# Kernel optimization log

Hardware: AMD Instinct MI355X
Metric: run time of the kernel (lower is better)

The kernel has to match this reference:

```python
import jax, jax.numpy as jnp
import numpy as np

N = 256          # num agents
HID = 128        # hidden_dim
ACT = 5          # action_dim
NH = 4           # num_heads
D = HID + 16     # concat_hidden_dim = 144
E = D * NH       # mha embed dim = 576
HD = D           # per-head dim = E // NH = 144
OBS_RX, OBS_RY = 4, 2   # obs_r from fov_size=(9,5)
GRID = 40


def setup_inputs() -> dict:
    key = jax.random.key(0)
    ks = jax.random.split(key, 24)
    g = lambda k, shape, s: (jax.random.normal(k, shape, dtype=jnp.float32) * s)
    inp = {
        "hidden_state_n": g(ks[0], (N, HID), 1.0),
        "action_n": g(ks[1], (N, HID), 1.0),
        "state_n": jax.random.randint(ks[2], (N, 2), 0, GRID, dtype=jnp.int32),
        # obs encoder
        "W_enc": g(ks[3], (HID, 16), HID ** -0.5), "b_enc": jnp.zeros((16,), jnp.float32),
        # MHABlock outer projections
        "Wq": g(ks[4], (D, E), D ** -0.5), "bq": jnp.zeros((E,), jnp.float32),
        "Wk": g(ks[5], (D, E), D ** -0.5), "bk": jnp.zeros((E,), jnp.float32),
        "Wv": g(ks[6], (D, E), D ** -0.5), "bv": jnp.zeros((E,), jnp.float32),
        # nn.MultiheadAttention internal in/out projections
        "Wiq": g(ks[7], (E, E), E ** -0.5), "biq": jnp.zeros((E,), jnp.float32),
        "Wik": g(ks[8], (E, E), E ** -0.5), "bik": jnp.zeros((E,), jnp.float32),
        "Wiv": g(ks[9], (E, E), E ** -0.5), "biv": jnp.zeros((E,), jnp.float32),
        "Wo_proj": g(ks[10], (E, E), E ** -0.5), "bo_proj": jnp.zeros((E,), jnp.float32),
        "W_O": g(ks[11], (E, D), E ** -0.5),  # no bias
        # dueling decoders
        "W_val": g(ks[12], (D, 1), D ** -0.5), "b_val": jnp.zeros((1,), jnp.float32),
        "W_adv": g(ks[13], (D, ACT), D ** -0.5), "b_adv": jnp.zeros((ACT,), jnp.float32),
    }
    return inp


def reference(hidden_state_n, action_n, W_enc, b_enc, Wq, bq, Wk, bk, Wv, bv,
              Wiq, biq, Wik, bik, Wiv, biv, Wo_proj, bo_proj, W_O,
              W_val, b_val, W_adv, b_adv, state_n):
    n = hidden_state_n.shape[0]
    # observed_agents[i] = {j > i : |x_i-x_j|<=rx and |y_i-y_j|<=ry}
    pos = state_n.astype(jnp.int32)
    dx = jnp.abs(pos[:, None, 0] - pos[None, :, 0])
    dy = jnp.abs(pos[:, None, 1] - pos[None, :, 1])
    upper = jnp.arange(n)[None, :] > jnp.arange(n)[:, None]
    mask = (dx <= OBS_RX) & (dy <= OBS_RY) & upper            # [N,N], mask[i,j]: j observed by i

    # per-neighbor feature c_j = concat(obs_encoder(h_j), a_j)  -> [N, D]
    obs = hidden_state_n @ W_enc + b_enc                       # [N,16]
    C = jnp.concatenate([obs, action_n], axis=-1)              # [N,D]

    # MHABlock: outer Q/K/V projections then nn.MultiheadAttention
    q = (C @ Wq + bq) @ Wiq + biq                              # [N,E]
    k = (C @ Wk + bk) @ Wik + bik
    v = (C @ Wv + bv) @ Wiv + biv
    q2 = q.reshape(n, NH, HD)
    k2 = k.reshape(n, NH, HD)
    v2 = v.reshape(n, NH, HD)

    scale = 1.0 / np.sqrt(HD).astype(np.float32)
    S = jnp.einsum("jhd,khd->hjk", q2, k2) * scale             # [H,N,N] shared across agents

    pair = (mask[:, None, :, None] & mask[:, None, None, :])   # [N,1,Nq,Nk]
    logits = jnp.where(pair, S[None, :, :, :], -1e9)           # [N,H,N,N]
    m = jnp.max(logits, axis=-1, keepdims=True)
    p = jnp.exp(logits - m) * pair.astype(logits.dtype)
    attn = p / jnp.maximum(p.sum(axis=-1, keepdims=True), 1e-9)

    ctx = jnp.einsum("ihjk,khd->ijhd", attn, v2).reshape(n, n, E)  # [N,Nq,E]
    out = (ctx @ Wo_proj + bo_proj) @ W_O                          # [N,Nq,D]

    # sum over the (masked) neighbor/query axis -> per-agent h_i
    h = jnp.sum(out * mask[:, :, None].astype(out.dtype), axis=1)  # [N,D]

    V = h @ W_val + b_val                                          # [N,1]
    A = h @ W_adv + b_adv                                          # [N,ACT]
    Q = V + A - jnp.mean(A, axis=-1, keepdims=True)                # dueling Q
    return Q
```

## Files before the change

kernel.cpp:

```cpp
#include <hip/hip_runtime.h>
#include <hip/hip_bf16.h>

#define NAG 256
#define HID 128
#define ACT 5
#define NH 4
#define DD 144
#define EE 576
#define HDIM 144
#define CMAX 20

__device__ __forceinline__ void prod_tile(
    const float* __restrict__ A, const float* __restrict__ W,
    float* __restrict__ out, int rowbase, int colbase, int N,
    int tid, float* sm)
{
    const int LDA = 580;
    float* As = sm;
    for (int idx = tid; idx < 8 * 144; idx += 256) {
        int r = idx / 144, c = idx % 144;
        *((float4*)&As[r * LDA + c * 4]) =
            *(const float4*)(A + (size_t)(rowbase + r) * 576 + c * 4);
    }
    __syncthreads();
    const int wave = tid >> 6, lane = tid & 63;
    const int colg = colbase + lane;
    const int colc = (colg < N) ? colg : (N - 1);
    const float* Wp = W + (size_t)(wave * 144) * N + colc;
    float acc[8] = {};
    float wv[36], wn[36];
    #pragma unroll
    for (int j = 0; j < 36; ++j) wv[j] = Wp[(size_t)j * N];
    for (int gi = 0; gi < 4; ++gi) {
        if (gi + 1 < 4) {
            const float* Wn = Wp + (size_t)(gi + 1) * 36 * N;
            #pragma unroll
            for (int j = 0; j < 36; ++j) wn[j] = Wn[(size_t)j * N];
        }
        const int kb = wave * 144 + gi * 36;
        #pragma unroll
        for (int j4 = 0; j4 < 9; ++j4) {
            #pragma unroll
            for (int r = 0; r < 8; ++r) {
                float4 a4 = *(const float4*)&As[r * LDA + kb + j4 * 4];
                acc[r] += a4.x * wv[j4 * 4 + 0] + a4.y * wv[j4 * 4 + 1]
                        + a4.z * wv[j4 * 4 + 2] + a4.w * wv[j4 * 4 + 3];
            }
        }
        #pragma unroll
        for (int j = 0; j < 36; ++j) wv[j] = wn[j];
    }
    __syncthreads();
    float* red = sm;
    #pragma unroll
    for (int r = 0; r < 8; ++r) red[wave * 512 + r * 64 + lane] = acc[r];
    __syncthreads();
    #pragma unroll
    for (int q = 0; q < 2; ++q) {
        int idx = tid + q * 256;
        int r = idx >> 6, cl = idx & 63;
        int col = colbase + cl;
        if (col < N) {
            float s = red[idx] + red[512 + idx] + red[1024 + idx] + red[1536 + idx];
            out[(size_t)(rowbase + r) * N + col] = s;
        }
    }
}

__global__ __launch_bounds__(256) void k_pre(
    const float* __restrict__ hidden, const float* __restrict__ action,
    const float* __restrict__ W_enc, const float* __restrict__ b_enc,
    const float* __restrict__ Wq, const float* __restrict__ Wk, const float* __restrict__ Wv,
    const float* __restrict__ bq, const float* __restrict__ bk, const float* __restrict__ bv,
    const float* __restrict__ Wiq, const float* __restrict__ Wik, const float* __restrict__ Wiv,
    const float* __restrict__ biq, const float* __restrict__ bik, const float* __restrict__ biv,
    const float* __restrict__ Wo, const float* __restrict__ bo, const float* __restrict__ W_O,
    float* __restrict__ C,
    float* __restrict__ Wqc, float* __restrict__ Wkc, float* __restrict__ Wvc,
    float* __restrict__ Wc,
    float* __restrict__ bqc, float* __restrict__ bkc, float* __restrict__ bvc,
    float* __restrict__ bvec)
{
    __shared__ float sm[4640];
    const int p = blockIdx.x, tid = threadIdx.x;
    if (p < 576) {
        const int xcd = p & 7, r = p >> 3;
        const int gslot = r / 18, mb = r % 18;
        const int g = xcd + 8 * gslot;
        if (g >= 27) return;
        const int bx = g % 9, z = g / 9;
        const float* A = (z == 0) ? Wq  : (z == 1) ? Wk  : Wv;
        const float* W = (z == 0) ? Wiq : (z == 1) ? Wik : Wiv;
        float*     out = (z == 0) ? Wqc : (z == 1) ? Wkc : Wvc;
        prod_tile(A, W, out, mb * 8, bx * 64, EE, tid, sm);
    } else if (p < 1152) {
        const int pp = p - 576;
        const int xcd = pp & 7, mb = pp >> 3;
        if (xcd >= 3) return;
        prod_tile(Wo, W_O, Wc, mb * 8, xcd * 64, DD, tid, sm);
    } else if (p < 1184) {
        const int mb = p - 1152;
        float* Hs = sm;
        float* We = sm + 1056;
        {
            int r = tid >> 5, kq = tid & 31;
            *((float4*)&Hs[r * 132 + kq * 4]) =
                *(const float4*)(hidden + (mb * 8 + r) * HID + kq * 4);
            float4 a4 = *(const float4*)(action + (mb * 8 + r) * HID + kq * 4);
            *((float4*)(C + (size_t)(mb * 8 + r) * DD + 16 + kq * 4)) = a4;
            *((float4*)&We[tid * 4])        = *(const float4*)(W_enc + tid * 4);
            *((float4*)&We[1024 + tid * 4]) = *(const float4*)(W_enc + 1024 + tid * 4);
        }
        __syncthreads();
        if (tid < 128) {
            int r = tid >> 4, o = tid & 15;
            float acc = 0.f;
            #pragma unroll 8
            for (int d = 0; d < HID; ++d) acc += Hs[r * 132 + d] * We[d * 16 + o];
            C[(size_t)(mb * 8 + r) * DD + o] = acc + b_enc[o];
        }
    } else {
        const int t = p - 1184;
        const float *bsel, *W, *badd;
        float* out;
        int N, bx;
        if (t < 27) {
            int z = t / 9; bx = t % 9; N = EE;
            bsel = (z == 0) ? bq  : (z == 1) ? bk  : bv;
            W    = (z == 0) ? Wiq : (z == 1) ? Wik : Wiv;
            badd = (z == 0) ? biq : (z == 1) ? bik : biv;
            out  = (z == 0) ? bqc : (z == 1) ? bkc : bvc;
        } else {
            bx = t - 27; N = DD;
            bsel = bo; W = W_O; badd = nullptr; out = bvec;
        }
        float* bs = sm;
        float* red = sm + 576;
        for (int i = tid; i < 144; i += 256)
            *((float4*)&bs[i * 4]) = *(const float4*)(bsel + i * 4);
        __syncthreads();
        const int wave = tid >> 6, lane = tid & 63;
        const int colg = bx * 64 + lane;
        const int colc = (colg < N) ? colg : (N - 1);
        float acc = 0.f;
        for (int k = wave * 144; k < wave * 144 + 144; ++k)
            acc += bs[k] * W[(size_t)k * N + colc];
        red[wave * 64 + lane] = acc;
        __syncthreads();
        if (tid < 64 && bx * 64 + tid < N) {
            float s = red[tid] + red[64 + tid] + red[128 + tid] + red[192 + tid];
            out[bx * 64 + tid] = s + (badd ? badd[bx * 64 + tid] : 0.f);
        }
    }
}

__global__ __launch_bounds__(256) void k_qkv(
    const float* __restrict__ C,
    const float* __restrict__ Wqc, const float* __restrict__ Wkc, const float* __restrict__ Wvc,
    const float* __restrict__ bqc, const float* __restrict__ bkc, const float* __restrict__ bvc,
    float* __restrict__ q, float* __restrict__ kb, float* __restrict__ v)
{
    const int p = blockIdx.x;
    const int xcd = p & 7, qq = p >> 3;
    const int mb = qq & 31, gslot = qq >> 5;
    const int g = xcd + 8 * gslot;
    if (g >= 27) return;
    const int bx = g % 9, z = g / 9;
    const float* W  = (z == 0) ? Wqc : (z == 1) ? Wkc : Wvc;
    const float* bi = (z == 0) ? bqc : (z == 1) ? bkc : bvc;
    float*      out = (z == 0) ? q   : (z == 1) ? kb  : v;
    const int tid = threadIdx.x;

    __shared__ union { float As[8 * 148]; float red[2048]; } u;
    for (int idx = tid; idx < 8 * 36; idx += 256) {
        int r = idx / 36, c = idx % 36;
        *((float4*)&u.As[r * 148 + c * 4]) =
            *(const float4*)(C + (size_t)(mb * 8 + r) * DD + c * 4);
    }
    __syncthreads();
    const int wave = tid >> 6, lane = tid & 63;
    const int colg = bx * 64 + lane;
    const float* Wp = W + (size_t)(wave * 36) * EE + colg;
    float acc[8] = {};
    float wv[36];
    #pragma unroll
    for (int j = 0; j < 36; ++j) wv[j] = Wp[(size_t)j * EE];
    const int kbase = wave * 36;
    #pragma unroll
    for (int j4 = 0; j4 < 9; ++j4) {
        #pragma unroll
        for (int r = 0; r < 8; ++r) {
            float4 a4 = *(const float4*)&u.As[r * 148 + kbase + j4 * 4];
            acc[r] += a4.x * wv[j4 * 4 + 0] + a4.y * wv[j4 * 4 + 1]
                    + a4.z * wv[j4 * 4 + 2] + a4.w * wv[j4 * 4 + 3];
        }
    }
    __syncthreads();
    #pragma unroll
    for (int r = 0; r < 8; ++r) u.red[wave * 512 + r * 64 + lane] = acc[r];
    __syncthreads();
    #pragma unroll
    for (int qi = 0; qi < 2; ++qi) {
        int idx = tid + qi * 256;
        int r = idx >> 6, cl = idx & 63;
        int col = bx * 64 + cl;
        float s = u.red[idx] + u.red[512 + idx]
                + u.red[1024 + idx] + u.red[1536 + idx];
        out[(size_t)(mb * 8 + r) * EE + col] = s + bi[col];
    }
}

__global__ __launch_bounds__(256) void k_attn(
    const int* __restrict__ state, const float* __restrict__ q,
    const float* __restrict__ kmat, const float* __restrict__ v,
    float* __restrict__ ctxsum, float* __restrict__ cnt)
{
    __shared__ int lst[NAG];
    __shared__ int cnt_s;
    __shared__ float w4[NH][NAG];
    __shared__ float qh[CMAX][HDIM + 1];
    __shared__ float kh[CMAX][HDIM + 1];
    __shared__ float Sl[CMAX][CMAX + 1];
    const int i = blockIdx.x, tid = threadIdx.x;
    if (tid == 0) cnt_s = 0;
    __syncthreads();
    {
        int xi = state[2 * i], yi = state[2 * i + 1];
        int xj = state[2 * tid], yj = state[2 * tid + 1];
        int dx = xi - xj; if (dx < 0) dx = -dx;
        int dy = yi - yj; if (dy < 0) dy = -dy;
        if (tid > i && dx <= 4 && dy <= 2) {
            int p = atomicAdd(&cnt_s, 1);
            lst[p] = tid;
        }
    }
    __syncthreads();
    const int c = cnt_s;
    if (tid == 0) cnt[i] = (float)c;
    if (c == 0) {
        for (int e = tid; e < EE; e += 256) ctxsum[i * EE + e] = 0.f;
        return;
    }
    if (c <= CMAX) {
        for (int h = 0; h < NH; ++h) {
            for (int idx = tid; idx < c * HDIM; idx += 256) {
                int jj = idx / HDIM, d = idx % HDIM;
                qh[jj][d] = q[lst[jj] * EE + h * HDIM + d];
                kh[jj][d] = kmat[lst[jj] * EE + h * HDIM + d];
            }
            __syncthreads();
            for (int pp = tid; pp < c * c; pp += 256) {
                int jj = pp / c, kk = pp % c;
                float acc = 0.f;
                for (int d = 0; d < HDIM; ++d) acc += qh[jj][d] * kh[kk][d];
                Sl[jj][kk] = acc * (1.0f / 12.0f);
            }
            __syncthreads();
            if (tid < c) {
                float m = -1e30f;
                for (int kk = 0; kk < c; ++kk) m = fmaxf(m, Sl[tid][kk]);
                float zz = 0.f;
                for (int kk = 0; kk < c; ++kk) zz += __expf(Sl[tid][kk] - m);
                float inv = 1.f / fmaxf(zz, 1e-9f);
                for (int kk = 0; kk < c; ++kk)
                    Sl[tid][kk] = __expf(Sl[tid][kk] - m) * inv;
            }
            __syncthreads();
            if (tid < c) {
                float s = 0.f;
                for (int jj = 0; jj < c; ++jj) s += Sl[jj][tid];
                w4[h][tid] = s;
            }
            __syncthreads();
        }
    } else {
        for (int idx = tid; idx < NH * c; idx += 256) w4[idx / c][idx % c] = 0.f;
        __syncthreads();
        for (int pnh = tid; pnh < NH * c; pnh += 256) {
            int h = pnh / c, jj = pnh % c;
            const float* qrow = q + lst[jj] * EE + h * HDIM;
            float m = -1e30f;
            for (int kk = 0; kk < c; ++kk) {
                const float* krow = kmat + lst[kk] * EE + h * HDIM;
                float a = 0.f;
                for (int d = 0; d < HDIM; ++d) a += qrow[d] * krow[d];
                m = fmaxf(m, a * (1.0f / 12.0f));
            }
            float zz = 0.f;
            for (int kk = 0; kk < c; ++kk) {
                const float* krow = kmat + lst[kk] * EE + h * HDIM;
                float a = 0.f;
                for (int d = 0; d < HDIM; ++d) a += qrow[d] * krow[d];
                zz += __expf(a * (1.0f / 12.0f) - m);
            }
            float inv = 1.f / fmaxf(zz, 1e-9f);
            for (int kk = 0; kk < c; ++kk) {
                const float* krow = kmat + lst[kk] * EE + h * HDIM;
                float a = 0.f;
                for (int d = 0; d < HDIM; ++d) a += qrow[d] * krow[d];
                atomicAdd(&w4[h][kk], __expf(a * (1.0f / 12.0f) - m) * inv);
            }
        }
        __syncthreads();
    }
    for (int e = tid; e < EE; e += 256) {
        int h = e / HDIM;
        float a0 = 0.f, a1 = 0.f;
        int t = 0;
        for (; t + 1 < c; t += 2) {
            a0 += w4[h][t] * v[lst[t] * EE + e];
            a1 += w4[h][t + 1] * v[lst[t + 1] * EE + e];
        }
        if (t < c) a0 += w4[h][t] * v[lst[t] * EE + e];
        ctxsum[i * EE + e] = a0 + a1;
    }
}

__global__ __launch_bounds__(256) void k_tail(
    const float* __restrict__ ctx, const float* __restrict__ Wc,
    const float* __restrict__ cnt, const float* __restrict__ bvec,
    const float* __restrict__ W_val, const float* __restrict__ b_val,
    const float* __restrict__ W_adv, const float* __restrict__ b_adv,
    float* __restrict__ out)
{
    __shared__ float As[4][EE];
    __shared__ float hb[4][DD];
    const int b = blockIdx.x, tid = threadIdx.x;
    const int a0 = b * 4;
    for (int idx = tid; idx < 4 * (EE / 4); idx += 256) {
        int r = idx / (EE / 4), c4 = idx % (EE / 4);
        *((float4*)&As[r][c4 * 4]) =
            *(const float4*)(ctx + (size_t)(a0 + r) * EE + c4 * 4);
    }
    __syncthreads();
    if (tid < DD) {
        const int col = tid;
        const float* Wp = Wc + col;
        float ac0 = 0.f, ac1 = 0.f, ac2 = 0.f, ac3 = 0.f;
        float wv[32], wn[32];
        #pragma unroll
        for (int j = 0; j < 32; ++j) wv[j] = Wp[(size_t)j * DD];
        for (int gI = 0; gI < 18; ++gI) {
            if (gI + 1 < 18) {
                const float* Wn = Wp + (size_t)(gI + 1) * 32 * DD;
                #pragma unroll
                for (int j = 0; j < 32; ++j) wn[j] = Wn[(size_t)j * DD];
            }
            const int kbase = gI * 32;
            #pragma unroll
            for (int j = 0; j < 32; ++j) {
                float w = wv[j];
                ac0 += As[0][kbase + j] * w; ac1 += As[1][kbase + j] * w;
                ac2 += As[2][kbase + j] * w; ac3 += As[3][kbase + j] * w;
            }
            #pragma unroll
            for (int j = 0; j < 32; ++j) wv[j] = wn[j];
        }
        float bvc = bvec[col];
        hb[0][col] = ac0 + cnt[a0 + 0] * bvc;
        hb[1][col] = ac1 + cnt[a0 + 1] * bvc;
        hb[2][col] = ac2 + cnt[a0 + 2] * bvc;
        hb[3][col] = ac3 + cnt[a0 + 3] * bvc;
    }
    __syncthreads();
    const int wave = tid >> 6, lane = tid & 63;
    float h0 = hb[wave][lane], h1 = hb[wave][lane + 64];
    float h2 = (lane < 16) ? hb[wave][lane + 128] : 0.f;
    float red[6];
    for (int o = 0; o < 6; ++o) {
        float p;
        if (o < 5) {
            p = h0 * W_adv[lane * ACT + o] + h1 * W_adv[(lane + 64) * ACT + o];
            if (lane < 16) p += h2 * W_adv[(lane + 128) * ACT + o];
        } else {
            p = h0 * W_val[lane] + h1 * W_val[lane + 64];
            if (lane < 16) p += h2 * W_val[lane + 128];
        }
        for (int off = 32; off; off >>= 1) p += __shfl_xor(p, off);
        red[o] = p;
    }
    if (lane == 0) {
        float a[ACT], mean = 0.f;
        for (int o = 0; o < ACT; ++o) { a[o] = red[o] + b_adv[o]; mean += a[o]; }
        mean *= (1.0f / ACT);
        float V = red[5] + b_val[0];
        for (int o = 0; o < ACT; ++o) out[(a0 + wave) * ACT + o] = V + a[o] - mean;
    }
}

extern "C" void kernel_launch(void* const* d_in, const int* in_sizes, int n_in,
                              void* d_out, int out_size, void* d_ws, size_t ws_size,
                              hipStream_t stream)
{
    const float* hidden = (const float*)d_in[0];
    const float* action = (const float*)d_in[1];
    const int*   state  = (const int*)d_in[2];

    float* ws = (float*)d_ws;
    float* C    = ws;
    float* Wqc  = C    + NAG * DD;
    float* Wkc  = Wqc  + DD * EE;
    float* Wvc  = Wkc  + DD * EE;
    float* Wc   = Wvc  + DD * EE;
    float* bqc  = Wc   + EE * DD;
    float* bkc  = bqc  + EE;
    float* bvc  = bkc  + EE;
    float* bvec = bvc  + EE;
    float* q    = bvec + DD;
    float* kb   = q    + NAG * EE;
    float* v    = kb   + NAG * EE;
    float* ctx  = v    + NAG * EE;
    float* cnt  = ctx  + NAG * EE;

    k_pre<<<1214, 256, 0, stream>>>(hidden, action,
        (const float*)d_in[3], (const float*)d_in[4],
        (const float*)d_in[5], (const float*)d_in[7], (const float*)d_in[9],
        (const float*)d_in[6], (const float*)d_in[8], (const float*)d_in[10],
        (const float*)d_in[11], (const float*)d_in[13], (const float*)d_in[15],
        (const float*)d_in[12], (const float*)d_in[14], (const float*)d_in[16],
        (const float*)d_in[17], (const float*)d_in[18], (const float*)d_in[19],
        C, Wqc, Wkc, Wvc, Wc, bqc, bkc, bvc, bvec);

    k_qkv<<<1024, 256, 0, stream>>>(C, Wqc, Wkc, Wvc, bqc, bkc, bvc, q, kb, v);

    k_attn<<<NAG, 256, 0, stream>>>(state, q, kb, v, ctx, cnt);

    k_tail<<<64, 256, 0, stream>>>(ctx, Wc, cnt, bvec,
        (const float*)d_in[20], (const float*)d_in[21],
        (const float*)d_in[22], (const float*)d_in[23], (float*)d_out);
}
```

Before: 193.2 us.

## Fuse all four stages into one cooperative persistent kernel with grid syncs

Replaces the four separate launches (weight pre-combination, QKV projection, attention, tail) with a single cooperative kernel. The kernel loops over work tiles per phase and separates phases with grid-wide syncs, and the attention and tail stages are merged per agent so ctx no longer round-trips through global memory. It also shrinks the register prefetch chunk in prod_tile from 36 to 24 and caps occupancy via launch_bounds(256,4). The aim is to remove inter-kernel launch gaps and tail idle time, at the cost of fewer resident blocks and grid-sync overhead. A fallback to the old four-kernel path is kept.

```diff
diff --git a/kernel.cpp b/kernel.cpp
--- a/kernel.cpp
+++ b/kernel.cpp
@@ -1,5 +1,7 @@
 #include <hip/hip_runtime.h>
-#include <hip/hip_bf16.h>
+#include <hip/hip_cooperative_groups.h>
+
+namespace cg = cooperative_groups;
 
 #define NAG 256
 #define HID 128
@@ -9,11 +11,12 @@
 #define EE 576
 #define HDIM 144
 #define CMAX 20
+#define COOP_GRID_MAX 768
 
 __device__ __forceinline__ void prod_tile(
     const float* __restrict__ A, const float* __restrict__ W,
     float* __restrict__ out, int rowbase, int colbase, int N,
-    int tid, float* sm)
+    int tid, float* __restrict__ sm)
 {
     const int LDA = 580;
     float* As = sm;
@@ -28,27 +31,27 @@
     const int colc = (colg < N) ? colg : (N - 1);
     const float* Wp = W + (size_t)(wave * 144) * N + colc;
     float acc[8] = {};
-    float wv[36], wn[36];
+    float wv[24], wn[24];
     #pragma unroll
-    for (int j = 0; j < 36; ++j) wv[j] = Wp[(size_t)j * N];
-    for (int gi = 0; gi < 4; ++gi) {
-        if (gi + 1 < 4) {
-            const float* Wn = Wp + (size_t)(gi + 1) * 36 * N;
+    for (int j = 0; j < 24; ++j) wv[j] = Wp[(size_t)j * N];
+    for (int gi = 0; gi < 6; ++gi) {
+        if (gi + 1 < 6) {
+            const float* Wn = Wp + (size_t)(gi + 1) * 24 * N;
             #pragma unroll
-            for (int j = 0; j < 36; ++j) wn[j] = Wn[(size_t)j * N];
-        }
-        const int kb = wave * 144 + gi * 36;
+            for (int j = 0; j < 24; ++j) wn[j] = Wn[(size_t)j * N];
+        }
+        const int kbase = wave * 144 + gi * 24;
         #pragma unroll
-        for (int j4 = 0; j4 < 9; ++j4) {
+        for (int j4 = 0; j4 < 6; ++j4) {
             #pragma unroll
             for (int r = 0; r < 8; ++r) {
-                float4 a4 = *(const float4*)&As[r * LDA + kb + j4 * 4];
+                float4 a4 = *(const float4*)&As[r * LDA + kbase + j4 * 4];
                 acc[r] += a4.x * wv[j4 * 4 + 0] + a4.y * wv[j4 * 4 + 1]
                         + a4.z * wv[j4 * 4 + 2] + a4.w * wv[j4 * 4 + 3];
             }
         }
         #pragma unroll
-        for (int j = 0; j < 36; ++j) wv[j] = wn[j];
+        for (int j = 0; j < 24; ++j) wv[j] = wn[j];
     }
     __syncthreads();
     float* red = sm;
@@ -56,14 +59,298 @@
     for (int r = 0; r < 8; ++r) red[wave * 512 + r * 64 + lane] = acc[r];
     __syncthreads();
     #pragma unroll
-    for (int q = 0; q < 2; ++q) {
-        int idx = tid + q * 256;
+    for (int qq = 0; qq < 2; ++qq) {
+        int idx = tid + qq * 256;
         int r = idx >> 6, cl = idx & 63;
         int col = colbase + cl;
         if (col < N) {
             float s = red[idx] + red[512 + idx] + red[1024 + idx] + red[1536 + idx];
             out[(size_t)(rowbase + r) * N + col] = s;
         }
+    }
+}
+
+__global__ __launch_bounds__(256, 4) void k_fused(
+    const float* __restrict__ hidden, const float* __restrict__ action,
+    const int* __restrict__ state,
+    const float* __restrict__ W_enc, const float* __restrict__ b_enc,
+    const float* __restrict__ Wq, const float* __restrict__ bq,
+    const float* __restrict__ Wk, const float* __restrict__ bk,
+    const float* __restrict__ Wv, const float* __restrict__ bv,
+    const float* __restrict__ Wiq, const float* __restrict__ biq,
+    const float* __restrict__ Wik, const float* __restrict__ bik,
+    const float* __restrict__ Wiv, const float* __restrict__ biv,
+    const float* __restrict__ Wo, const float* __restrict__ bo,
+    const float* __restrict__ W_O,
+    const float* __restrict__ W_val, const float* __restrict__ b_val,
+    const float* __restrict__ W_adv, const float* __restrict__ b_adv,
+    float* __restrict__ C,
+    float* __restrict__ Wqc, float* __restrict__ Wkc, float* __restrict__ Wvc,
+    float* __restrict__ Wc,
+    float* __restrict__ bqc, float* __restrict__ bkc, float* __restrict__ bvc,
+    float* __restrict__ bvec,
+    float* __restrict__ q, float* __restrict__ kb, float* __restrict__ v,
+    float* __restrict__ out)
+{
+    __shared__ float smf[7504];
+    const int bid = blockIdx.x, tid = threadIdx.x;
+    const int gsz = gridDim.x;
+    cg::grid_group gg = cg::this_grid();
+
+    for (int t = bid; t < 764; t += gsz) {
+        if (t < 486) {
+            const int g = t / 18, mb = t % 18;
+            const int z = g / 9, bx = g % 9;
+            const float* A = (z == 0) ? Wq  : (z == 1) ? Wk  : Wv;
+            const float* W = (z == 0) ? Wiq : (z == 1) ? Wik : Wiv;
+            float*     o   = (z == 0) ? Wqc : (z == 1) ? Wkc : Wvc;
+            prod_tile(A, W, o, mb * 8, bx * 64, EE, tid, smf);
+        } else if (t < 702) {
+            const int s = t - 486;
+            const int mb = s / 3, bx = s % 3;
+            prod_tile(Wo, W_O, Wc, mb * 8, bx * 64, DD, tid, smf);
+        } else if (t < 734) {
+            const int mb = t - 702;
+            float* Hs = smf;
+            float* We = smf + 1056;
+            {
+                int r = tid >> 5, kq = tid & 31;
+                *((float4*)&Hs[r * 132 + kq * 4]) =
+                    *(const float4*)(hidden + (mb * 8 + r) * HID + kq * 4);
+                float4 a4 = *(const float4*)(action + (mb * 8 + r) * HID + kq * 4);
+                *((float4*)(C + (size_t)(mb * 8 + r) * DD + 16 + kq * 4)) = a4;
+                *((float4*)&We[tid * 4])        = *(const float4*)(W_enc + tid * 4);
+                *((float4*)&We[1024 + tid * 4]) = *(const float4*)(W_enc + 1024 + tid * 4);
+            }
+            __syncthreads();
+            if (tid < 128) {
+                int r = tid >> 4, o = tid & 15;
+                float acc = 0.f;
+                #pragma unroll 8
+                for (int d = 0; d < HID; ++d) acc += Hs[r * 132 + d] * We[d * 16 + o];
+                C[(size_t)(mb * 8 + r) * DD + o] = acc + b_enc[o];
+            }
+        } else {
+            const int tt = t - 734;
+            const float *bsel, *W, *badd;
+            float* o;
+            int N, bx;
+            if (tt < 27) {
+                int z = tt / 9; bx = tt % 9; N = EE;
+                bsel = (z == 0) ? bq  : (z == 1) ? bk  : bv;
+                W    = (z == 0) ? Wiq : (z == 1) ? Wik : Wiv;
+                badd = (z == 0) ? biq : (z == 1) ? bik : biv;
+                o    = (z == 0) ? bqc : (z == 1) ? bkc : bvc;
+            } else {
+                bx = tt - 27; N = DD;
+                bsel = bo; W = W_O; badd = nullptr; o = bvec;
+            }
+            float* bs = smf;
+            float* red = smf + 576;
+            for (int i2 = tid; i2 < 144; i2 += 256)
+                *((float4*)&bs[i2 * 4]) = *(const float4*)(bsel + i2 * 4);
+            __syncthreads();
+            const int wave = tid >> 6, lane = tid & 63;
+            const int colg = bx * 64 + lane;
+            const int colc = (colg < N) ? colg : (N - 1);
+            float acc = 0.f;
+            for (int k = wave * 144; k < wave * 144 + 144; ++k)
+                acc += bs[k] * W[(size_t)k * N + colc];
+            red[wave * 64 + lane] = acc;
+            __syncthreads();
+            if (tid < 64 && bx * 64 + tid < N) {
+                float s = red[tid] + red[64 + tid] + red[128 + tid] + red[192 + tid];
+                o[bx * 64 + tid] = s + (badd ? badd[bx * 64 + tid] : 0.f);
+            }
+        }
+        __syncthreads();
+    }
+    __threadfence();
+    gg.sync();
+
+    for (int t = bid; t < 864; t += gsz) {
+        const int g = t / 32, mb = t % 32;
+        const int z = g / 9, bx = g % 9;
+        const float* W  = (z == 0) ? Wqc : (z == 1) ? Wkc : Wvc;
+        const float* bi = (z == 0) ? bqc : (z == 1) ? bkc : bvc;
+        float*     outp = (z == 0) ? q   : (z == 1) ? kb  : v;
+        for (int idx = tid; idx < 8 * 36; idx += 256) {
+            int r = idx / 36, cc = idx % 36;
+            *((float4*)&smf[r * 148 + cc * 4]) =
+                *(const float4*)(C + (size_t)(mb * 8 + r) * DD + cc * 4);
+        }
+        __syncthreads();
+        const int wave = tid >> 6, lane = tid & 63;
+        const int colg = bx * 64 + lane;
+        const float* Wp = W + (size_t)(wave * 36) * EE + colg;
+        float acc[8] = {};
+        float wv[36];
+        #pragma unroll
+        for (int j = 0; j < 36; ++j) wv[j] = Wp[(size_t)j * EE];
+        const int kbase = wave * 36;
+        #pragma unroll
+        for (int j4 = 0; j4 < 9; ++j4) {
+            #pragma unroll
+            for (int r = 0; r < 8; ++r) {
+                float4 a4 = *(const float4*)&smf[r * 148 + kbase + j4 * 4];
+                acc[r] += a4.x * wv[j4 * 4 + 0] + a4.y * wv[j4 * 4 + 1]
+                        + a4.z * wv[j4 * 4 + 2] + a4.w * wv[j4 * 4 + 3];
+            }
+        }
+        __syncthreads();
+        #pragma unroll
+        for (int r = 0; r < 8; ++r) smf[wave * 512 + r * 64 + lane] = acc[r];
+        __syncthreads();
+        #pragma unroll
+        for (int qi = 0; qi < 2; ++qi) {
+            int idx = tid + qi * 256;
+            int r = idx >> 6, cl = idx & 63;
+            int col = bx * 64 + cl;
+            float s = smf[idx] + smf[512 + idx] + smf[1024 + idx] + smf[1536 + idx];
+            outp[(size_t)(mb * 8 + r) * EE + col] = s + bi[col];
+        }
+        __syncthreads();
+    }
+    __threadfence();
+    gg.sync();
+
+    for (int i = bid; i < NAG; i += gsz) {
+        int*  lst  = (int*)smf;
+        int*  cnts = (int*)(smf + 256);
+        float* w4f = smf + 260;
+        float (*qh)[HDIM + 1] = (float(*)[HDIM + 1])(smf + 1284);
+        float (*kh)[HDIM + 1] = (float(*)[HDIM + 1])(smf + 4184);
+        float (*Sl)[CMAX + 1] = (float(*)[CMAX + 1])(smf + 7084);
+        float* ctxs = smf + 1284;
+        float* hs   = smf + 1860;
+
+        if (tid == 0) *cnts = 0;
+        __syncthreads();
+        {
+            int xi = state[2 * i], yi = state[2 * i + 1];
+            int xj = state[2 * tid], yj = state[2 * tid + 1];
+            int dx = xi - xj; if (dx < 0) dx = -dx;
+            int dy = yi - yj; if (dy < 0) dy = -dy;
+            if (tid > i && dx <= 4 && dy <= 2) {
+                int p = atomicAdd(cnts, 1);
+                lst[p] = tid;
+            }
+        }
+        __syncthreads();
+        const int c = *cnts;
+        if (c > 0 && c <= CMAX) {
+            for (int h = 0; h < NH; ++h) {
+                for (int idx = tid; idx < c * HDIM; idx += 256) {
+                    int jj = idx / HDIM, d = idx % HDIM;
+                    qh[jj][d] = q[lst[jj] * EE + h * HDIM + d];
+                    kh[jj][d] = kb[lst[jj] * EE + h * HDIM + d];
+                }
+                __syncthreads();
+                for (int pp = tid; pp < c * c; pp += 256) {
+                    int jj = pp / c, kk = pp % c;
+                    float acc = 0.f;
+                    for (int d = 0; d < HDIM; ++d) acc += qh[jj][d] * kh[kk][d];
+                    Sl[jj][kk] = acc * (1.0f / 12.0f);
+                }
+                __syncthreads();
+                if (tid < c) {
+                    float m = -1e30f;
+                    for (int kk = 0; kk < c; ++kk) m = fmaxf(m, Sl[tid][kk]);
+                    float zz = 0.f;
+                    for (int kk = 0; kk < c; ++kk) zz += __expf(Sl[tid][kk] - m);
+                    float inv = 1.f / fmaxf(zz, 1e-9f);
+                    for (int kk = 0; kk < c; ++kk)
+                        Sl[tid][kk] = __expf(Sl[tid][kk] - m) * inv;
+                }
+                __syncthreads();
+                if (tid < c) {
+                    float s = 0.f;
+                    for (int jj = 0; jj < c; ++jj) s += Sl[jj][tid];
+                    w4f[h * NAG + tid] = s;
+                }
+                __syncthreads();
+            }
+        } else if (c > CMAX) {
+            for (int idx = tid; idx < NH * c; idx += 256)
+                w4f[(idx / c) * NAG + (idx % c)] = 0.f;
+            __syncthreads();
+            for (int pnh = tid; pnh < NH * c; pnh += 256) {
+                int h = pnh / c, jj = pnh % c;
+                const float* qrow = q + lst[jj] * EE + h * HDIM;
+                float m = -1e30f;
+                for (int kk = 0; kk < c; ++kk) {
+                    const float* krow = kb + lst[kk] * EE + h * HDIM;
+                    float a = 0.f;
+                    for (int d = 0; d < HDIM; ++d) a += qrow[d] * krow[d];
+                    m = fmaxf(m, a * (1.0f / 12.0f));
+                }
+                float zz = 0.f;
+                for (int kk = 0; kk < c; ++kk) {
+                    const float* krow = kb + lst[kk] * EE + h * HDIM;
+                    float a = 0.f;
+                    for (int d = 0; d < HDIM; ++d) a += qrow[d] * krow[d];
+                    zz += __expf(a * (1.0f / 12.0f) - m);
+                }
+                float inv = 1.f / fmaxf(zz, 1e-9f);
+                for (int kk = 0; kk < c; ++kk) {
+                    const float* krow = kb + lst[kk] * EE + h * HDIM;
+                    float a = 0.f;
+                    for (int d = 0; d < HDIM; ++d) a += qrow[d] * krow[d];
+                    atomicAdd(&w4f[h * NAG + kk], __expf(a * (1.0f / 12.0f) - m) * inv);
+                }
+            }
+            __syncthreads();
+        }
+        if (c > 0) {
+            for (int e = tid; e < EE; e += 256) {
+                int h = e / HDIM;
+                float a0 = 0.f, a1 = 0.f;
+                int t2 = 0;
+                for (; t2 + 1 < c; t2 += 2) {
+                    a0 += w4f[h * NAG + t2] * v[lst[t2] * EE + e];
+                    a1 += w4f[h * NAG + t2 + 1] * v[lst[t2 + 1] * EE + e];
+                }
+                if (t2 < c) a0 += w4f[h * NAG + t2] * v[lst[t2] * EE + e];
+                ctxs[e] = a0 + a1;
+            }
+        }
+        __syncthreads();
+        if (tid < DD) {
+            float acc = 0.f;
+            if (c > 0) {
+                const float* Wp = Wc + tid;
+                #pragma unroll 8
+                for (int k2 = 0; k2 < EE; ++k2) acc += ctxs[k2] * Wp[(size_t)k2 * DD];
+            }
+            hs[tid] = acc + (float)c * bvec[tid];
+        }
+        __syncthreads();
+        if (tid < 64) {
+            const int lane = tid;
+            float h0 = hs[lane], h1 = hs[lane + 64];
+            float h2 = (lane < 16) ? hs[lane + 128] : 0.f;
+            float red6[6];
+            for (int o = 0; o < 6; ++o) {
+                float p2;
+                if (o < 5) {
+                    p2 = h0 * W_adv[lane * ACT + o] + h1 * W_adv[(lane + 64) * ACT + o];
+                    if (lane < 16) p2 += h2 * W_adv[(lane + 128) * ACT + o];
+                } else {
+                    p2 = h0 * W_val[lane] + h1 * W_val[lane + 64];
+                    if (lane < 16) p2 += h2 * W_val[lane + 128];
+                }
+                for (int off = 32; off; off >>= 1) p2 += __shfl_xor(p2, off);
+                red6[o] = p2;
+            }
+            if (lane == 0) {
+                float a[ACT], mean = 0.f;
+                for (int o = 0; o < ACT; ++o) { a[o] = red6[o] + b_adv[o]; mean += a[o]; }
+                mean *= (1.0f / ACT);
+                float V = red6[5] + b_val[0];
+                for (int o = 0; o < ACT; ++o) out[i * ACT + o] = V + a[o] - mean;
+            }
+        }
+        __syncthreads();
     }
 }
 
@@ -392,10 +679,6 @@
                               void* d_out, int out_size, void* d_ws, size_t ws_size,
                               hipStream_t stream)
 {
-    const float* hidden = (const float*)d_in[0];
-    const float* action = (const float*)d_in[1];
-    const int*   state  = (const int*)d_in[2];
-
     float* ws = (float*)d_ws;
     float* C    = ws;
     float* Wqc  = C    + NAG * DD;
@@ -412,20 +695,78 @@
     float* ctx  = v    + NAG * EE;
     float* cnt  = ctx  + NAG * EE;
 
-    k_pre<<<1214, 256, 0, stream>>>(hidden, action,
-        (const float*)d_in[3], (const float*)d_in[4],
-        (const float*)d_in[5], (const float*)d_in[7], (const float*)d_in[9],
-        (const float*)d_in[6], (const float*)d_in[8], (const float*)d_in[10],
-        (const float*)d_in[11], (const float*)d_in[13], (const float*)d_in[15],
-        (const float*)d_in[12], (const float*)d_in[14], (const float*)d_in[16],
-        (const float*)d_in[17], (const float*)d_in[18], (const float*)d_in[19],
-        C, Wqc, Wkc, Wvc, Wc, bqc, bkc, bvc, bvec);
-
-    k_qkv<<<1024, 256, 0, stream>>>(C, Wqc, Wkc, Wvc, bqc, bkc, bvc, q, kb, v);
-
-    k_attn<<<NAG, 256, 0, stream>>>(state, q, kb, v, ctx, cnt);
-
-    k_tail<<<64, 256, 0, stream>>>(ctx, Wc, cnt, bvec,
-        (const float*)d_in[20], (const float*)d_in[21],
-        (const float*)d_in[22], (const float*)d_in[23], (float*)d_out);
+    const float* hidden = (const float*)d_in[0];
+    const float* action = (const float*)d_in[1];
+    const int*   state  = (const int*)d_in[2];
+    const float* W_enc  = (const float*)d_in[3];
+    const float* b_enc  = (const float*)d_in[4];
+    const float* Wq     = (const float*)d_in[5];
+    const float* bq     = (const float*)d_in[6];
+    const float* Wk     = (const float*)d_in[7];
+    const float* bk     = (const float*)d_in[8];
+    const float* Wv     = (const float*)d_in[9];
+    const float* bv     = (const float*)d_in[10];
+    const float* Wiq    = (const float*)d_in[11];
+    const float* biq    = (const float*)d_in[12];
+    const float* Wik    = (const float*)d_in[13];
+    const float* bik    = (const float*)d_in[14];
+    const float* Wiv    = (const float*)d_in[15];
+    const float* biv    = (const float*)d_in[16];
+    const float* Wo     = (const float*)d_in[17];
+    const float* bo     = (const float*)d_in[18];
+    const float* W_O    = (const float*)d_in[19];
+    const float* W_val  = (const float*)d_in[20];
+    const float* b_val  = (const float*)d_in[21];
+    const float* W_adv  = (const float*)d_in[22];
+    const float* b_adv  = (const float*)d_in[23];
+    float* outp = (float*)d_out;
+
+    static int coop_grid = 0;
+    if (coop_grid == 0) {
+        int perCU = 0;
+        hipError_t e1 = hipOccupancyMaxActiveBlocksPerMultiprocessor(
+            &perCU, k_fused, 256, 0);
+        hipDeviceProp_t prop;
+        int dev = 0;
+        hipGetDevice(&dev);
+        hipError_t e2 = hipGetDeviceProperties(&prop, dev);
+        if (e1 == hipSuccess && e2 == hipSuccess && perCU > 0) {
+            long cap = (long)perCU * (long)prop.multiProcessorCount;
+            coop_grid = (int)((cap < COOP_GRID_MAX) ? cap : COOP_GRID_MAX);
+        } else {
+            coop_grid = -1;
+        }
+    }
+
+    bool done = false;
+    if (coop_grid > 0) {
+        void* args[] = {
+            (void*)&hidden, (void*)&action, (void*)&state,
+            (void*)&W_enc, (void*)&b_enc,
+            (void*)&Wq, (void*)&bq, (void*)&Wk, (void*)&bk, (void*)&Wv, (void*)&bv,
+            (void*)&Wiq, (void*)&biq, (void*)&Wik, (void*)&bik, (void*)&Wiv, (void*)&biv,
+            (void*)&Wo, (void*)&bo, (void*)&W_O,
+            (void*)&W_val, (void*)&b_val, (void*)&W_adv, (void*)&b_adv,
+            (void*)&C, (void*)&Wqc, (void*)&Wkc, (void*)&Wvc, (void*)&Wc,
+            (void*)&bqc, (void*)&bkc, (void*)&bvc, (void*)&bvec,
+            (void*)&q, (void*)&kb, (void*)&v, (void*)&outp
+        };
+        hipError_t le = hipLaunchCooperativeKernel(
+            k_fused, dim3(coop_grid), dim3(256), args, 0, stream);
+        if (le == hipSuccess) {
+            done = true;
+        } else {
+            coop_grid = -1;
+        }
+    }
+
+    if (!done) {
+        k_pre<<<1214, 256, 0, stream>>>(hidden, action, W_enc, b_enc,
+            Wq, Wk, Wv, bq, bk, bv, Wiq, Wik, Wiv, biq, bik, biv,
+            Wo, bo, W_O, C, Wqc, Wkc, Wvc, Wc, bqc, bkc, bvc, bvec);
+        k_qkv<<<1024, 256, 0, stream>>>(C, Wqc, Wkc, Wvc, bqc, bkc, bvc, q, kb, v);
+        k_attn<<<NAG, 256, 0, stream>>>(state, q, kb, v, ctx, cnt);
+        k_tail<<<64, 256, 0, stream>>>(ctx, Wc, cnt, bvec,
+            W_val, b_val, W_adv, b_adv, outp);
+    }
 }
```

Result: slower. 417.3 us (+116.0%).
